# Kernel optimization log

Measured on AMD Instinct MI355X. Metric: run time of the kernel, lower is better.

The kernel has to match this reference:

```python
import jax, jax.numpy as jnp
import numpy as np

D, H, F, Z = 768, 12, 2048, 100   # d_model, nhead, dim_feedforward, d_z
NL = 2                            # num enc layers == num dec layers
RATIO = 0.05                      # filter_ratio
EPS = 1e-5


def _ln(x, g, b):
    m = x.mean(-1, keepdims=True)
    v = ((x - m) ** 2).mean(-1, keepdims=True)
    return (x - m) / jnp.sqrt(v + EPS) * g + b


def _mha(x, bias, qkv_w, qkv_b, out_w, out_b):
    # x: [N, L, D] (torch seq-first: seq=N responses, batch=L token positions)
    # bias: [L, N] float key-padding mask, ADDED to logits (torch float-mask semantics)
    N, L, _ = x.shape
    hd = D // H
    qkv = jnp.einsum('nld,ed->nle', x, qkv_w) + qkv_b
    q, k, v = jnp.split(qkv, 3, axis=-1)
    q = q.reshape(N, L, H, hd)
    k = k.reshape(N, L, H, hd)
    v = v.reshape(N, L, H, hd)
    scores = jnp.einsum('nlhd,mlhd->lhnm', q, k) / jnp.sqrt(jnp.float32(hd))
    scores = scores + bias[:, None, None, :]
    attn = jax.nn.softmax(scores, axis=-1)
    o = jnp.einsum('lhnm,mlhd->nlhd', attn, v).reshape(N, L, D)
    return o @ out_w.T + out_b


def _stack(x, bias, p):
    qkv_w, qkv_b, out_w, out_b, g1, b1, w1, c1, w2, c2, g2, b2 = p
    for i in range(NL):  # post-norm TransformerEncoderLayer, relu FFN, eval (no dropout)
        a = _mha(x, bias, qkv_w[i], qkv_b[i], out_w[i], out_b[i])
        x = _ln(x + a, g1[i], b1[i])
        f = jax.nn.relu(x @ w1[i].T + c1[i]) @ w2[i].T + c2[i]
        x = _ln(x + f, g2[i], b2[i])
    return x


def _anomaly_scores(emb, msk, enc_p, dec_p, pe_w, pe_b, pd_w, pd_b):
    bias = msk.T  # [L, N]
    h = _stack(emb, bias, enc_p)
    z = jnp.tanh(h @ pe_w.T + pe_b)
    zd = jnp.tanh(z @ pd_w.T + pd_b)
    d = _stack(zd, bias, dec_p)
    # per-response MSE between mean decoded and mean input embedding, summed over D
    return ((d.mean(axis=1) - emb.mean(axis=1)) ** 2).sum(-1)


def _forward(tree_lens, inputs_embeds, attention_mask, enc_p, dec_p, pe_w, pe_b, pd_w, pd_b):
    B, T, L, _ = inputs_embeds.shape
    tls = np.asarray(tree_lens)
    n_resp = tls - 1
    # pack ragged replies: rows 1..tree_len-1 of every tree -> [Ntot, L, D]
    b_idx = np.concatenate([np.full(n, b) for b, n in enumerate(n_resp)])
    t_idx = np.concatenate([np.arange(1, tl) for tl in tls])
    reply = inputs_embeds[b_idx, t_idx]
    masks = attention_mask[b_idx, t_idx]
    s = _anomaly_scores(reply, masks, enc_p, dec_p, pe_w, pe_b, pd_w, pd_b)  # [Ntot]
    Ntot = s.shape[0]
    # original: rank_idx = global_argsort filtered to indices < n_resp[b] (min is always 0)
    # == argsort of the FIRST n_resp[b] packed scores (faithful to the source's indexing)
    masked = jnp.where(jnp.arange(Ntot)[None, :] < jnp.asarray(n_resp)[:, None],
                       s[None, :], jnp.inf)
    order = jnp.argsort(masked, axis=1)[:, :T - 1]  # [B, T-1]
    n_ext = np.maximum(np.floor(n_resp * RATIO).astype(np.int64), 1)
    sel = np.arange(T - 1)[None, :] < n_ext[:, None]          # [B, T-1]
    selj = jnp.asarray(sel)
    node_idx = jnp.where(selj, order + 1, 0)                  # pad slots reuse src (node 0)
    node_full = jnp.concatenate([jnp.zeros((B, 1), node_idx.dtype), node_idx], axis=1)
    brow = jnp.arange(B)[:, None]
    new_emb = inputs_embeds[brow, node_full]                  # [B, T, L, D]
    valid = jnp.asarray(np.concatenate([np.ones((B, 1), bool), sel], axis=1)
                        ).astype(attention_mask.dtype)
    new_msk = attention_mask[brow, node_full] * valid[:, :, None]  # pad rows get zero mask
    ohidx = jnp.where(selj, order + 1, T)                     # dump masked scatters to col T
    oh = jnp.zeros((B, T + 1), jnp.int32).at[brow, ohidx].set(1)[:, :T].at[:, 0].set(1)
    ext_mask = jnp.repeat(oh[:, :, None], L, axis=2).reshape(B, T * L)
    new_tree_lens = jnp.asarray(1 + n_ext, dtype=jnp.int32)
    n_ext_adv = 0
    return oh, ext_mask, n_ext_adv, new_tree_lens, new_emb, new_msk


def setup_inputs() -> dict:
    B, T, L = 16, 32, 64
    key = jax.random.key(0)
    ks = list(jax.random.split(key, 4))
    inp = {
        'tree_lens': jax.random.randint(ks[0], (B,), T // 2, T + 1),
        'inputs_embeds': jax.random.normal(ks[1], (B, T, L, D), jnp.float32),
        'attention_mask': jnp.ones((B, T, L), jnp.float32),
    }
    kit = iter(jax.random.split(ks[2], 32))
    def w(shape):
        return jax.random.normal(next(kit), (NL,) + shape, jnp.float32) * 0.02
    for pre in ('enc', 'dec'):
        inp[pre + '_qkv_w'] = w((3 * D, D)); inp[pre + '_qkv_b'] = jnp.zeros((NL, 3 * D))
        inp[pre + '_out_w'] = w((D, D));     inp[pre + '_out_b'] = jnp.zeros((NL, D))
        inp[pre + '_ln1_g'] = jnp.ones((NL, D)); inp[pre + '_ln1_b'] = jnp.zeros((NL, D))
        inp[pre + '_w1'] = w((F, D)); inp[pre + '_c1'] = jnp.zeros((NL, F))
        inp[pre + '_w2'] = w((D, F)); inp[pre + '_c2'] = jnp.zeros((NL, D))
        inp[pre + '_ln2_g'] = jnp.ones((NL, D)); inp[pre + '_ln2_b'] = jnp.zeros((NL, D))
    inp['pe_w'] = jax.random.normal(next(kit), (Z, D), jnp.float32) * 0.02
    inp['pe_b'] = jnp.zeros((Z,), jnp.float32)
    inp['pd_w'] = jax.random.normal(next(kit), (D, Z), jnp.float32) * 0.02
    inp['pd_b'] = jnp.zeros((D,), jnp.float32)
    return inp


def reference(tree_lens, inputs_embeds, attention_mask,
              enc_qkv_w, enc_qkv_b, enc_out_w, enc_out_b, enc_ln1_g, enc_ln1_b,
              enc_w1, enc_c1, enc_w2, enc_c2, enc_ln2_g, enc_ln2_b,
              dec_qkv_w, dec_qkv_b, dec_out_w, dec_out_b, dec_ln1_g, dec_ln1_b,
              dec_w1, dec_c1, dec_w2, dec_c2, dec_ln2_g, dec_ln2_b,
              pe_w, pe_b, pd_w, pd_b):
    enc_p = (enc_qkv_w, enc_qkv_b, enc_out_w, enc_out_b, enc_ln1_g, enc_ln1_b,
             enc_w1, enc_c1, enc_w2, enc_c2, enc_ln2_g, enc_ln2_b)
    dec_p = (dec_qkv_w, dec_qkv_b, dec_out_w, dec_out_b, dec_ln1_g, dec_ln1_b,
             dec_w1, dec_c1, dec_w2, dec_c2, dec_ln2_g, dec_ln2_b)
    return _forward(tree_lens, inputs_embeds, attention_mask, enc_p, dec_p,
                    pe_w, pe_b, pd_w, pd_b)
```

## Files before the change

kernel.cpp:

```cpp
#include <hip/hip_runtime.h>
#include <hip/hip_bf16.h>
#include <math.h>


#define B_  16
#define T_  32
#define L_  64
#define D_  768
#define H_  12
#define F_  2048
#define ZR_ 100
#define ZP_ 128
#define NP_ 512
#define EPS_ 1e-5f

#define MI_NTOT  0
#define MI_NRESP 8
#define MI_OFF   32
#define MI_BIDX  64
#define MI_TIDX  576
#define MI_NODE  1088

#define WS_BIAS2 2048
#define WS_EMEAN 34816
#define WS_S     428032
#define WS_WST   428544
#define WS_BIG   1313280

#define OUT_OH   0
#define OUT_EXT  512
#define OUT_NEA  33280
#define OUT_NTL  33281
#define OUT_NEMB 33297
#define OUT_NMSK 25199121
#define OUT_XSCR 33300

typedef __attribute__((ext_vector_type(8))) short short8;
typedef __attribute__((ext_vector_type(4))) float f32x4;

__device__ inline float bf2f(unsigned s) {
  return __uint_as_float((s & 0xffffu) << 16);
}
__device__ inline unsigned short f2bf(float x) {
  unsigned u = __float_as_uint(x);
  u += 0x7fffu + ((u >> 16) & 1u);
  return (unsigned short)(u >> 16);
}
__device__ inline unsigned pack2(float a, float b) {
  return (unsigned)f2bf(a) | ((unsigned)f2bf(b) << 16);
}

__global__ void meta_kernel(const int* __restrict__ tl, int* __restrict__ mi) {
  if (threadIdx.x != 0) return;
  int off = 0;
  for (int b = 0; b < B_; b++) {
    int nr = tl[b] - 1;
    mi[MI_NRESP + b] = nr;
    mi[MI_OFF + b] = off;
    off += nr;
  }
  mi[MI_NTOT] = off;
  for (int j = 0; j < NP_; j++) {
    int b = -1, t = 0;
    if (j < off) {
      b = 0;
      while (b + 1 < B_ && j >= mi[MI_OFF + b + 1]) b++;
      t = j - mi[MI_OFF + b] + 1;
    }
    mi[MI_BIDX + j] = b;
    mi[MI_TIDX + j] = t;
  }
}

__global__ __launch_bounds__(256) void w2bf_kernel(const float* __restrict__ W,
                                                   unsigned short* __restrict__ o) {
  const int i = (blockIdx.x * 256 + threadIdx.x) * 4;
  float4 v = *(const float4*)(W + i);
  uint2 pk; pk.x = pack2(v.x, v.y); pk.y = pack2(v.z, v.w);
  *(uint2*)(o + i) = pk;
}

__global__ __launch_bounds__(192) void gather_kernel(
    const float* __restrict__ emb, const float* __restrict__ am,
    const int* __restrict__ mi, unsigned short* __restrict__ X,
    float* __restrict__ bias2) {
  const int blk = blockIdx.x;
  const int j = blk >> 6, l = blk & 63;
  const int ntot = mi[MI_NTOT];
  const int t = threadIdx.x;
  float4 v = make_float4(0.f, 0.f, 0.f, 0.f);
  if (j < ntot) {
    const int b = mi[MI_BIDX + j], tt = mi[MI_TIDX + j];
    v = ((const float4*)(emb + (size_t)((b * T_ + tt) * L_ + l) * D_))[t];
    if (t == 0) bias2[blk] = am[(b * T_ + tt) * L_ + l];
  } else {
    if (t == 0) bias2[blk] = -1e30f;
  }
  uint2 pk; pk.x = pack2(v.x, v.y); pk.y = pack2(v.z, v.w);
  *(uint2*)(X + (size_t)blk * D_ + t * 4) = pk;
}

__global__ __launch_bounds__(256) void emean_kernel(const unsigned short* __restrict__ X,
                                                    float* __restrict__ em) {
  const int j = blockIdx.x;
  int d = threadIdx.x;
  for (int c = 0; c < 3; c++, d += 256) {
    const unsigned short* p = X + (size_t)j * L_ * D_ + d;
    float s = 0.f;
    for (int l = 0; l < L_; l++) s += bf2f(p[l * D_]);
    em[j * D_ + d] = s * (1.f / 64.f);
  }
}

__device__ inline float blockSum256(float v, float* red) {
  #pragma unroll
  for (int o = 32; o > 0; o >>= 1) v += __shfl_down(v, o);
  const int lane = threadIdx.x & 63, wid = threadIdx.x >> 6;
  __syncthreads();
  if (lane == 0) red[wid] = v;
  __syncthreads();
  return red[0] + red[1] + red[2] + red[3];
}

__global__ __launch_bounds__(256) void ln_kernel(unsigned short* __restrict__ X,
                                                 const float* __restrict__ g,
                                                 const float* __restrict__ bb,
                                                 const int* __restrict__ mi) {
  const int row = blockIdx.x * 4 + (threadIdx.x >> 6);
  if (row >= mi[MI_NTOT] * L_) return;
  const int lane = threadIdx.x & 63;
  unsigned short* p = X + (size_t)row * D_;
  float v[12];
  #pragma unroll
  for (int c = 0; c < 3; c++) {
    uint2 u = *(const uint2*)(p + lane * 4 + c * 256);
    v[c * 4 + 0] = bf2f(u.x); v[c * 4 + 1] = bf2f(u.x >> 16);
    v[c * 4 + 2] = bf2f(u.y); v[c * 4 + 3] = bf2f(u.y >> 16);
  }
  float s = 0.f;
  #pragma unroll
  for (int i = 0; i < 12; i++) s += v[i];
  #pragma unroll
  for (int o = 32; o > 0; o >>= 1) s += __shfl_xor(s, o);
  const float m = s * (1.f / 768.f);
  float q = 0.f;
  #pragma unroll
  for (int i = 0; i < 12; i++) { v[i] -= m; q += v[i] * v[i]; }
  #pragma unroll
  for (int o = 32; o > 0; o >>= 1) q += __shfl_xor(q, o);
  const float r = rsqrtf(q * (1.f / 768.f) + EPS_);
  #pragma unroll
  for (int c = 0; c < 3; c++) {
    const int d = lane * 4 + c * 256;
    float4 gv = *(const float4*)(g + d);
    float4 bv = *(const float4*)(bb + d);
    uint2 pk;
    pk.x = pack2(v[c * 4 + 0] * r * gv.x + bv.x, v[c * 4 + 1] * r * gv.y + bv.y);
    pk.y = pack2(v[c * 4 + 2] * r * gv.z + bv.z, v[c * 4 + 3] * r * gv.w + bv.w);
    *(uint2*)(p + d) = pk;
  }
}

template <int ACT, bool ADD>
__global__ __launch_bounds__(512) void gemm_mfma(
    const unsigned short* __restrict__ A, int lda, int K,
    const unsigned short* __restrict__ W, int ldw,
    const float* __restrict__ bias,
    unsigned short* __restrict__ C, int ldc,
    const int* __restrict__ mi) {
  const int rows = mi[MI_NTOT] * 64;
  const int row0 = blockIdx.x * 256;
  if (row0 >= rows) return;
  const int col0 = blockIdx.y * 256;
  __shared__ unsigned short Sh[6 * 8192];
  unsigned short* SA = Sh;
  unsigned short* SB = Sh + 3 * 8192;
  const int t = threadIdx.x;
  const int lane = t & 63, w = t >> 6;
  const int wr = w >> 2, wc = w & 3;
  const int quad = lane >> 4, l15 = lane & 15;
  f32x4 acc[8][4];
  #pragma unroll
  for (int i = 0; i < 8; i++)
    #pragma unroll
    for (int j = 0; j < 4; j++) acc[i][j] = (f32x4){0.f, 0.f, 0.f, 0.f};

  int schunk[2];
  const unsigned short* gA[2];
  const unsigned short* gB[2];
  #pragma unroll
  for (int r = 0; r < 2; r++) {
    const int c = r * 8 + w;
    const int g = c * 64 + lane;
    const int row = g >> 2, slot = g & 3;
    const int kg = slot ^ ((row >> 1) & 3);
    schunk[r] = c;
    gA[r] = A + (size_t)(row0 + row) * lda + kg * 8;
    gB[r] = W + (size_t)(col0 + row) * ldw + kg * 8;
  }
  int aoff[8], boff[4];
  #pragma unroll
  for (int m = 0; m < 8; m++) {
    const int ar = wr * 128 + m * 16 + l15;
    aoff[m] = ar * 32 + (quad ^ ((ar >> 1) & 3)) * 8;
  }
  #pragma unroll
  for (int n = 0; n < 4; n++) {
    const int bn = wc * 64 + n * 16 + l15;
    boff[n] = bn * 32 + (quad ^ ((bn >> 1) & 3)) * 8;
  }

#define STAGE_(bi_, kk_)                                                       \
  { const int _off = (bi_) * 8192;                                             \
    _Pragma("unroll")                                                          \
    for (int r = 0; r < 2; r++) {                                              \
      __builtin_amdgcn_global_load_lds(                                        \
          (const __attribute__((address_space(1))) void*)(gA[r] + (kk_)),      \
          (__attribute__((address_space(3))) void*)(SA + _off + schunk[r] * 512), \
          16, 0, 0);                                                           \
      __builtin_amdgcn_global_load_lds(                                        \
          (const __attribute__((address_space(1))) void*)(gB[r] + (kk_)),      \
          (__attribute__((address_space(3))) void*)(SB + _off + schunk[r] * 512), \
          16, 0, 0);                                                           \
    } }

#define COMPUTE_(bi_)                                                          \
  {                                                                            \
    const int _off = (bi_) * 8192;                                             \
    short8 bfr[4];                                                             \
    _Pragma("unroll")                                                          \
    for (int n = 0; n < 4; n++) bfr[n] = *(const short8*)(SB + _off + boff[n]); \
    _Pragma("unroll")                                                          \
    for (int m = 0; m < 8; m++) {                                              \
      short8 afm = *(const short8*)(SA + _off + aoff[m]);                      \
      _Pragma("unroll")                                                        \
      for (int n = 0; n < 4; n++)                                              \
        acc[m][n] = __builtin_amdgcn_mfma_f32_16x16x32_bf16(afm, bfr[n],       \
                                                            acc[m][n], 0, 0, 0); \
    }                                                                          \
  }

  const int NS = K >> 5;
  STAGE_(0, 0);
  STAGE_(1, 32);
  int bi = 0;
  for (int i = 0; i < NS; i++) {
    if (i + 1 < NS) {
      asm volatile("s_waitcnt vmcnt(4)\ns_barrier" ::: "memory");
    } else {
      asm volatile("s_waitcnt vmcnt(0)\ns_barrier" ::: "memory");
    }
    __builtin_amdgcn_sched_barrier(0);
    if (i + 2 < NS) {
      const int b2 = (bi >= 1) ? bi - 1 : 2;
      STAGE_(b2, (i + 2) * 32);
    }
    COMPUTE_(bi);
    bi = (bi >= 2) ? 0 : bi + 1;
  }
  __syncthreads();

#undef STAGE_
#undef COMPUTE_

  unsigned short* slice = Sh + w * 4096;
  float bv[4];
  #pragma unroll
  for (int n = 0; n < 4; n++) bv[n] = bias[col0 + wc * 64 + n * 16 + l15];
  #pragma unroll
  for (int p = 0; p < 2; p++) {
    #pragma unroll
    for (int mm = 0; mm < 4; mm++) {
      #pragma unroll
      for (int reg = 0; reg < 4; reg++) {
        const int r64 = mm * 16 + quad * 4 + reg;
        #pragma unroll
        for (int n = 0; n < 4; n++) {
          float x = acc[p * 4 + mm][n][reg] + bv[n];
          if (ACT == 1) x = fmaxf(x, 0.f);
          slice[r64 * 64 + n * 16 + l15] = f2bf(x);
        }
      }
    }
    unsigned short* crow =
        C + (size_t)(row0 + wr * 128 + p * 64) * ldc + col0 + wc * 64;
    #pragma unroll
    for (int i = 0; i < 8; i++) {
      const int j = i * 64 + lane;
      const int r64 = j >> 3, c8 = (j & 7) * 8;
      short8 v = *(const short8*)(slice + j * 8);
      unsigned short* cp = crow + (size_t)r64 * ldc + c8;
      if (ADD) {
        short8 cv = *(const short8*)cp;
        #pragma unroll
        for (int e = 0; e < 8; e++)
          v[e] = (short)f2bf(bf2f((unsigned short)v[e]) +
                             bf2f((unsigned short)cv[e]));
      }
      *(short8*)cp = v;
    }
  }
}

template <int ACT, int AT, int CT>
__global__ __launch_bounds__(256) void gemm_kernel(
    const void* __restrict__ Av, int lda, int kloop,
    const float* __restrict__ W, int kw, int nreal,
    const float* __restrict__ bias,
    void* __restrict__ Cv, int ldc,
    const int* __restrict__ mi) {
  if ((int)blockIdx.x >= mi[MI_NTOT]) return;
  __shared__ float As[16][68];
  __shared__ float Ws[16][68];
  const int t = threadIdx.x;
  const int tx = t & 15, ty = t >> 4;
  const int lrow = t >> 2, lkg = (t & 3) * 4;
  const size_t row0 = (size_t)blockIdx.x * 64;
  const int col0 = blockIdx.y * 64;
  float acc[4][4] = {};
  for (int k0 = 0; k0 < kloop; k0 += 16) {
    float a4[4];
    if (AT == 0) {
      float4 av = *(const float4*)((const float*)Av + (row0 + lrow) * (size_t)lda + k0 + lkg);
      a4[0] = av.x; a4[1] = av.y; a4[2] = av.z; a4[3] = av.w;
    } else {
      uint2 u = *(const uint2*)((const unsigned short*)Av + (row0 + lrow) * (size_t)lda + k0 + lkg);
      a4[0] = bf2f(u.x); a4[1] = bf2f(u.x >> 16);
      a4[2] = bf2f(u.y); a4[3] = bf2f(u.y >> 16);
    }
    float wv[4];
    const int wn = col0 + lrow;
    #pragma unroll
    for (int i = 0; i < 4; i++) {
      const int k = k0 + lkg + i;
      wv[i] = (wn < nreal && k < kw) ? W[(size_t)wn * kw + k] : 0.f;
    }
    __syncthreads();
    As[lkg + 0][lrow] = a4[0]; As[lkg + 1][lrow] = a4[1];
    As[lkg + 2][lrow] = a4[2]; As[lkg + 3][lrow] = a4[3];
    Ws[lkg + 0][lrow] = wv[0]; Ws[lkg + 1][lrow] = wv[1];
    Ws[lkg + 2][lrow] = wv[2]; Ws[lkg + 3][lrow] = wv[3];
    __syncthreads();
    #pragma unroll
    for (int kk = 0; kk < 16; kk++) {
      float4 av4 = *(const float4*)(&As[kk][ty * 4]);
      float4 wv4 = *(const float4*)(&Ws[kk][tx * 4]);
      float aa[4] = {av4.x, av4.y, av4.z, av4.w};
      float ww[4] = {wv4.x, wv4.y, wv4.z, wv4.w};
      #pragma unroll
      for (int i = 0; i < 4; i++)
        #pragma unroll
        for (int j = 0; j < 4; j++) acc[i][j] += aa[i] * ww[j];
    }
  }
  const int n0 = col0 + tx * 4;
  float bv[4];
  #pragma unroll
  for (int j = 0; j < 4; j++) bv[j] = (n0 + j < nreal) ? bias[n0 + j] : 0.f;
  #pragma unroll
  for (int i = 0; i < 4; i++) {
    float v[4];
    #pragma unroll
    for (int j = 0; j < 4; j++) {
      float x = acc[i][j] + bv[j];
      if (ACT == 1) x = fmaxf(x, 0.f);
      if (ACT == 2) x = tanhf(x);
      v[j] = x;
    }
    if (CT == 0) {
      float* cp = (float*)Cv + (row0 + ty * 4 + i) * (size_t)ldc + n0;
      *(float4*)cp = make_float4(v[0], v[1], v[2], v[3]);
    } else {
      unsigned short* cp = (unsigned short*)Cv + (row0 + ty * 4 + i) * (size_t)ldc + n0;
      uint2 pk; pk.x = pack2(v[0], v[1]); pk.y = pack2(v[2], v[3]);
      *(uint2*)cp = pk;
    }
  }
}

__global__ __launch_bounds__(512) void attn_kernel(
    unsigned short* __restrict__ QKV, const float* __restrict__ bias2,
    const int* __restrict__ mi) {
  const int ntot = mi[MI_NTOT];
  const int l = blockIdx.x, h = blockIdx.y;
  const int ntk = (ntot + 63) >> 6;
  __shared__ unsigned short Ks[512 * 64];
  __shared__ unsigned short Vt[8 * 4096];
  __shared__ unsigned short Ps[8][1024];
  __shared__ float bs[512];
  const int t = threadIdx.x;
  const int lane = t & 63, w = t >> 6;
  const int quad = lane >> 4, l15 = lane & 15;

  {
    const int sub = lane >> 3;
    const int cc = (lane & 7) ^ sub;
    for (int it = 0; it < ntk; it++) {
      const int m = it * 64 + w * 8 + sub;
      const unsigned short* src =
          QKV + (size_t)(m * L_ + l) * 2304 + 768 + h * 64 + cc * 8;
      __builtin_amdgcn_global_load_lds(
          (const __attribute__((address_space(1))) void*)src,
          (__attribute__((address_space(3))) void*)(Ks + it * 4096 + w * 512),
          16, 0, 0);
    }
  }
  {
    const int m = t & 63;
    const int d0 = (t >> 6) * 8;
    for (int mt = 0; mt < ntk; mt++) {
      short8 v = *(const short8*)(
          QKV + (size_t)((mt * 64 + m) * L_ + l) * 2304 + 1536 + h * 64 + d0);
      #pragma unroll
      for (int i = 0; i < 8; i++) {
        const int d = d0 + i;
        Vt[mt * 4096 + d * 64 + (((m >> 3) ^ (d & 7)) * 8) + (m & 7)] =
            (unsigned short)v[i];
      }
    }
  }
  bs[t] = bias2[t * 64 + l];
  __syncthreads();

  const int nqt = (ntot + 127) >> 7;
  for (int qt = 0; qt < nqt; qt++) {
    const int qbase = qt * 128 + w * 16;
    if (qbase >= ntot) continue;

    short8 af[2];
    #pragma unroll
    for (int kc = 0; kc < 2; kc++)
      af[kc] = *(const short8*)(
          QKV + (size_t)((qbase + l15) * L_ + l) * 2304 + h * 64 + (kc * 4 + quad) * 8);

    f32x4 oa[4];
    float runmax[4], runsum[4];
    #pragma unroll
    for (int f = 0; f < 4; f++) oa[f] = (f32x4){0.f, 0.f, 0.f, 0.f};
    #pragma unroll
    for (int r2 = 0; r2 < 4; r2++) { runmax[r2] = -3.0e38f; runsum[r2] = 0.f; }

    for (int mt = 0; mt < ntk; mt++) {
      f32x4 sv[4];
      #pragma unroll
      for (int cb = 0; cb < 4; cb++) {
        sv[cb] = (f32x4){0.f, 0.f, 0.f, 0.f};
        const int mrow = mt * 64 + cb * 16 + l15;
        #pragma unroll
        for (int kc = 0; kc < 2; kc++) {
          short8 bk = *(const short8*)(
              Ks + mrow * 64 + (((kc * 4 + quad) ^ (mrow & 7)) * 8));
          sv[cb] = __builtin_amdgcn_mfma_f32_16x16x32_bf16(af[kc], bk, sv[cb], 0, 0, 0);
        }
      }

      float bj[4];
      #pragma unroll
      for (int cb = 0; cb < 4; cb++) bj[cb] = bs[mt * 64 + cb * 16 + l15];
      float pj[4][4];
      #pragma unroll
      for (int cb = 0; cb < 4; cb++)
        #pragma unroll
        for (int r2 = 0; r2 < 4; r2++) pj[cb][r2] = sv[cb][r2] * 0.125f + bj[cb];
      float tmax[4];
      #pragma unroll
      for (int r2 = 0; r2 < 4; r2++)
        tmax[r2] = fmaxf(fmaxf(pj[0][r2], pj[1][r2]), fmaxf(pj[2][r2], pj[3][r2]));
      #pragma unroll
      for (int o2 = 1; o2 < 16; o2 <<= 1)
        #pragma unroll
        for (int r2 = 0; r2 < 4; r2++) tmax[r2] = fmaxf(tmax[r2], __shfl_xor(tmax[r2], o2));
      float tsum[4];
      #pragma unroll
      for (int r2 = 0; r2 < 4; r2++) {
        const float nmax = fmaxf(runmax[r2], tmax[r2]);
        const float alpha = __expf(runmax[r2] - nmax);
        runmax[r2] = nmax;
        float s0 = 0.f;
        #pragma unroll
        for (int cb = 0; cb < 4; cb++) { pj[cb][r2] = __expf(pj[cb][r2] - nmax); s0 += pj[cb][r2]; }
        tsum[r2] = s0;
        runsum[r2] *= alpha;
        #pragma unroll
        for (int f = 0; f < 4; f++) oa[f][r2] *= alpha;
      }
      #pragma unroll
      for (int o2 = 1; o2 < 16; o2 <<= 1)
        #pragma unroll
        for (int r2 = 0; r2 < 4; r2++) tsum[r2] += __shfl_xor(tsum[r2], o2);
      #pragma unroll
      for (int r2 = 0; r2 < 4; r2++) runsum[r2] += tsum[r2];

      #pragma unroll
      for (int cb = 0; cb < 4; cb++) {
        const int m = cb * 16 + l15;
        #pragma unroll
        for (int r2 = 0; r2 < 4; r2++) {
          const int q = quad * 4 + r2;
          Ps[w][q * 64 + (((m >> 3) ^ (q & 7)) * 8) + (m & 7)] = f2bf(pj[cb][r2]);
        }
      }
      short8 pa[2];
      #pragma unroll
      for (int kc = 0; kc < 2; kc++)
        pa[kc] = *(const short8*)(
            &Ps[w][l15 * 64 + (((kc * 4 + quad) ^ (l15 & 7)) * 8)]);
      #pragma unroll
      for (int f = 0; f < 4; f++) {
        const int d = f * 16 + l15;
        #pragma unroll
        for (int kc = 0; kc < 2; kc++) {
          short8 bv = *(const short8*)(
              Vt + mt * 4096 + d * 64 + (((kc * 4 + quad) ^ (d & 7)) * 8));
          oa[f] = __builtin_amdgcn_mfma_f32_16x16x32_bf16(pa[kc], bv, oa[f], 0, 0, 0);
        }
      }
    }

    #pragma unroll
    for (int r2 = 0; r2 < 4; r2++) {
      const float inv = 1.f / runsum[r2];
      const int q = quad * 4 + r2;
      #pragma unroll
      for (int f = 0; f < 4; f++)
        Ps[w][q * 64 + f * 16 + l15] = f2bf(oa[f][r2] * inv);
    }
    #pragma unroll
    for (int i = 0; i < 2; i++) {
      const int j = lane + i * 64;
      const int q = j >> 3, c8 = j & 7;
      short8 v = *(const short8*)(&Ps[w][j * 8]);
      *(short8*)(QKV + (size_t)((qbase + q) * L_ + l) * 2304 + h * 64 + c8 * 8) = v;
    }
  }
}

__global__ __launch_bounds__(256) void score_kernel(const unsigned short* __restrict__ X,
                                                    const float* __restrict__ em,
                                                    float* __restrict__ Sv) {
  const int j = blockIdx.x;
  const int t = threadIdx.x;
  __shared__ float red[4];
  float part = 0.f;
  for (int c = 0; c < 3; c++) {
    const int d = t + c * 256;
    const unsigned short* p = X + (size_t)j * L_ * D_ + d;
    float s = 0.f;
    for (int l = 0; l < L_; l++) s += bf2f(p[l * D_]);
    const float diff = s * (1.f / 64.f) - em[j * D_ + d];
    part += diff * diff;
  }
  const float tot = blockSum256(part, red);
  if (t == 0) Sv[j] = tot;
}

__global__ __launch_bounds__(256) void finalize_kernel(const float* __restrict__ Sv,
                                                       int* __restrict__ mi,
                                                       float* __restrict__ out) {
  const int t = threadIdx.x;
  if (t < B_) {
    const int nr = mi[MI_NRESP + t];
    float best = 3.0e38f; int bi = 0;
    for (int j = 0; j < nr; j++) {
      const float v = Sv[j];
      if (v < best) { best = v; bi = j; }
    }
    mi[MI_NODE + t] = bi + 1;
    int next = nr / 20; if (next < 1) next = 1;
    out[OUT_NTL + t] = (float)(1 + next);
  }
  if (t == 0) out[OUT_NEA] = 0.f;
  __syncthreads();
  for (int idx = t; idx < B_ * T_; idx += 256) {
    const int b = idx >> 5, tt = idx & 31;
    out[OUT_OH + idx] = (tt == 0 || tt == mi[MI_NODE + b]) ? 1.f : 0.f;
  }
}

__global__ __launch_bounds__(256) void maskout_kernel(const float* __restrict__ am,
                                                      const int* __restrict__ mi,
                                                      float* __restrict__ out) {
  const int idx = blockIdx.x * 256 + threadIdx.x;
  const int b = idx >> 11, rem = idx & 2047;
  const int tt = rem >> 6, l = rem & 63;
  const int node = mi[MI_NODE + b];
  out[OUT_EXT + idx] = (tt == 0 || tt == node) ? 1.f : 0.f;
  float nm;
  if (tt == 0)      nm = am[(b * T_) * L_ + l];
  else if (tt == 1) nm = am[(b * T_ + node) * L_ + l];
  else              nm = 0.f;
  out[OUT_NMSK + idx] = nm;
}

__global__ __launch_bounds__(192) void newemb_kernel(const float* __restrict__ emb,
                                                     const int* __restrict__ mi,
                                                     float* __restrict__ out) {
  const int blk = blockIdx.x;
  const int b = blk >> 11, rem = blk & 2047;
  const int tt = rem >> 6, l = rem & 63;
  const int srct = (tt == 1) ? mi[MI_NODE + b] : 0;
  const float4 v = ((const float4*)(emb + (size_t)((b * T_ + srct) * L_ + l) * D_))[threadIdx.x];
  float* dst = out + OUT_NEMB + (size_t)blk * D_ + threadIdx.x * 4;
  dst[0] = v.x; dst[1] = v.y; dst[2] = v.z; dst[3] = v.w;
}

extern "C" void kernel_launch(void* const* d_in, const int* in_sizes, int n_in,
                              void* d_out, int out_size, void* d_ws, size_t ws_size,
                              hipStream_t stream) {
  (void)in_sizes; (void)n_in; (void)out_size; (void)ws_size;
  const int*   tl  = (const int*)d_in[0];
  const float* emb = (const float*)d_in[1];
  const float* am  = (const float*)d_in[2];
  const float* P[28];
  for (int i = 0; i < 28; i++) P[i] = (const float*)d_in[3 + i];

  float* wsf   = (float*)d_ws;
  int*   mi    = (int*)d_ws;
  float* bias2 = wsf + WS_BIAS2;
  float* emean = wsf + WS_EMEAN;
  float* Sv    = wsf + WS_S;
  unsigned short* Wst = (unsigned short*)(wsf + WS_WST);
  unsigned short* BIG = (unsigned short*)(wsf + WS_BIG);
  float* Zb    = wsf + WS_BIG;
  float* out   = (float*)d_out;
  unsigned short* X = (unsigned short*)(out + OUT_XSCR);

  meta_kernel<<<1, 64, 0, stream>>>(tl, mi);
  gather_kernel<<<NP_ * L_, 192, 0, stream>>>(emb, am, mi, X, bias2);
  emean_kernel<<<NP_, 256, 0, stream>>>(X, emean);

  const int RTM = NP_ * 64 / 256;
  const int LNB = NP_ * L_ / 4;
  for (int s = 0; s < 2; s++) {
    const float* const* q = P + s * 12;
    for (int i = 0; i < 2; i++) {
      w2bf_kernel<<<(3 * D_ * D_) / 1024, 256, 0, stream>>>(q[0] + (size_t)i * 3 * D_ * D_, Wst);
      gemm_mfma<0, false><<<dim3(RTM, 9), 512, 0, stream>>>(
          X, D_, D_, Wst, D_, q[1] + i * 3 * D_, BIG, 3 * D_, mi);
      attn_kernel<<<dim3(L_, H_), 512, 0, stream>>>(BIG, bias2, mi);
      w2bf_kernel<<<(D_ * D_) / 1024, 256, 0, stream>>>(q[2] + (size_t)i * D_ * D_, Wst);
      gemm_mfma<0, true><<<dim3(RTM, 3), 512, 0, stream>>>(
          BIG, 3 * D_, D_, Wst, D_, q[3] + i * D_, X, D_, mi);
      ln_kernel<<<LNB, 256, 0, stream>>>(X, q[4] + i * D_, q[5] + i * D_, mi);
      w2bf_kernel<<<(F_ * D_) / 1024, 256, 0, stream>>>(q[6] + (size_t)i * F_ * D_, Wst);
      gemm_mfma<1, false><<<dim3(RTM, 8), 512, 0, stream>>>(
          X, D_, D_, Wst, D_, q[7] + i * F_, BIG, F_, mi);
      w2bf_kernel<<<(D_ * F_) / 1024, 256, 0, stream>>>(q[8] + (size_t)i * D_ * F_, Wst);
      gemm_mfma<0, true><<<dim3(RTM, 3), 512, 0, stream>>>(
          BIG, F_, F_, Wst, F_, q[9] + i * D_, X, D_, mi);
      ln_kernel<<<LNB, 256, 0, stream>>>(X, q[10] + i * D_, q[11] + i * D_, mi);
    }
    if (s == 0) {
      gemm_kernel<2, 1, 0><<<dim3(NP_, 2), 256, 0, stream>>>(
          X, D_, D_, P[24], D_, ZR_, P[25], Zb, ZP_, mi);
      gemm_kernel<2, 0, 1><<<dim3(NP_, 12), 256, 0, stream>>>(
          Zb, ZP_, ZP_, P[26], ZR_, D_, P[27], X, D_, mi);
    }
  }

  score_kernel<<<NP_, 256, 0, stream>>>(X, emean, Sv);
  finalize_kernel<<<1, 256, 0, stream>>>(Sv, mi, out);
  maskout_kernel<<<128, 256, 0, stream>>>(am, mi, out);
  newemb_kernel<<<B_ * T_ * L_, 192, 0, stream>>>(emb, mi, out);
}
```

Measured before the change: 2.376 ms.

## Restructure MFMA GEMM main loop to K=64 double-buffered phased pipeline

The bf16 GEMM main loop moves from a triple-buffered K=32 scheme to a double-buffered K=64 tile with an XOR-swizzled LDS layout. Each iteration is split into four phases that issue one slice of next-tile global-to-LDS loads, read A/B fragments, then run an MFMA burst under raised wave priority (s_setprio), with barriers between phases. The aim is finer interleaving of memory traffic and matrix work with fewer loop iterations and less barrier overhead per FLOP. In exchange it uses more LDS (128KB) and adds extra barriers per iteration.

```diff
diff --git a/kernel.cpp b/kernel.cpp
--- a/kernel.cpp
+++ b/kernel.cpp
@@ -172,9 +172,7 @@
   const int row0 = blockIdx.x * 256;
   if (row0 >= rows) return;
   const int col0 = blockIdx.y * 256;
-  __shared__ unsigned short Sh[6 * 8192];
-  unsigned short* SA = Sh;
-  unsigned short* SB = Sh + 3 * 8192;
+  __shared__ unsigned short Sh[2 * 32768];
   const int t = threadIdx.x;
   const int lane = t & 63, w = t >> 6;
   const int wr = w >> 2, wc = w & 3;
@@ -185,83 +183,88 @@
     #pragma unroll
     for (int j = 0; j < 4; j++) acc[i][j] = (f32x4){0.f, 0.f, 0.f, 0.f};
 
-  int schunk[2];
-  const unsigned short* gA[2];
-  const unsigned short* gB[2];
-  #pragma unroll
-  for (int r = 0; r < 2; r++) {
-    const int c = r * 8 + w;
-    const int g = c * 64 + lane;
-    const int row = g >> 2, slot = g & 3;
-    const int kg = slot ^ ((row >> 1) & 3);
-    schunk[r] = c;
-    gA[r] = A + (size_t)(row0 + row) * lda + kg * 8;
-    gB[r] = W + (size_t)(col0 + row) * ldw + kg * 8;
-  }
-  int aoff[8], boff[4];
-  #pragma unroll
-  for (int m = 0; m < 8; m++) {
-    const int ar = wr * 128 + m * 16 + l15;
-    aoff[m] = ar * 32 + (quad ^ ((ar >> 1) & 3)) * 8;
-  }
-  #pragma unroll
-  for (int n = 0; n < 4; n++) {
-    const int bn = wc * 64 + n * 16 + l15;
-    boff[n] = bn * 32 + (quad ^ ((bn >> 1) & 3)) * 8;
-  }
-
-#define STAGE_(bi_, kk_)                                                       \
-  { const int _off = (bi_) * 8192;                                             \
+  const int sr  = w * 8 + (lane >> 3);
+  const int cc8 = ((lane & 7) ^ (lane >> 3)) * 8;
+
+  int aoffm[8], boffn[4];
+  #pragma unroll
+  for (int m = 0; m < 8; m++) aoffm[m] = (wr * 128 + m * 16 + l15) * 64;
+  #pragma unroll
+  for (int n = 0; n < 4; n++) boffn[n] = (wc * 64 + n * 16 + l15) * 64;
+  const int e7 = l15 & 7;
+  const int pq0 = ((quad)     ^ e7) * 8;
+  const int pq1 = ((4 + quad) ^ e7) * 8;
+
+#define STG(bi_, mat_, h_, kt_)                                                \
+  { const unsigned short* gp_ = (mat_) ? W : A;                                \
+    const int ld_ = (mat_) ? ldw : lda;                                        \
+    const int b0_ = (mat_) ? col0 : row0;                                      \
     _Pragma("unroll")                                                          \
-    for (int r = 0; r < 2; r++) {                                              \
+    for (int j_ = 0; j_ < 2; j_++) {                                           \
+      const unsigned short* src_ =                                             \
+          gp_ + (size_t)(b0_ + (h_) * 128 + j_ * 64 + sr) * ld_ +              \
+          (kt_) * 64 + cc8;                                                    \
       __builtin_amdgcn_global_load_lds(                                        \
-          (const __attribute__((address_space(1))) void*)(gA[r] + (kk_)),      \
-          (__attribute__((address_space(3))) void*)(SA + _off + schunk[r] * 512), \
-          16, 0, 0);                                                           \
-      __builtin_amdgcn_global_load_lds(                                        \
-          (const __attribute__((address_space(1))) void*)(gB[r] + (kk_)),      \
-          (__attribute__((address_space(3))) void*)(SB + _off + schunk[r] * 512), \
+          (const __attribute__((address_space(1))) void*)src_,                 \
+          (__attribute__((address_space(3))) void*)(Sh + (bi_) * 32768 +       \
+              (mat_) * 16384 + (h_) * 8192 + j_ * 4096 + w * 512),             \
           16, 0, 0);                                                           \
     } }
 
-#define COMPUTE_(bi_)                                                          \
-  {                                                                            \
-    const int _off = (bi_) * 8192;                                             \
-    short8 bfr[4];                                                             \
-    _Pragma("unroll")                                                          \
-    for (int n = 0; n < 4; n++) bfr[n] = *(const short8*)(SB + _off + boff[n]); \
-    _Pragma("unroll")                                                          \
-    for (int m = 0; m < 8; m++) {                                              \
-      short8 afm = *(const short8*)(SA + _off + aoff[m]);                      \
-      _Pragma("unroll")                                                        \
-      for (int n = 0; n < 4; n++)                                              \
-        acc[m][n] = __builtin_amdgcn_mfma_f32_16x16x32_bf16(afm, bfr[n],       \
-                                                            acc[m][n], 0, 0, 0); \
-    }                                                                          \
-  }
-
-  const int NS = K >> 5;
-  STAGE_(0, 0);
-  STAGE_(1, 32);
-  int bi = 0;
-  for (int i = 0; i < NS; i++) {
-    if (i + 1 < NS) {
-      asm volatile("s_waitcnt vmcnt(4)\ns_barrier" ::: "memory");
-    } else {
-      asm volatile("s_waitcnt vmcnt(0)\ns_barrier" ::: "memory");
-    }
-    __builtin_amdgcn_sched_barrier(0);
-    if (i + 2 < NS) {
-      const int b2 = (bi >= 1) ? bi - 1 : 2;
-      STAGE_(b2, (i + 2) * 32);
-    }
-    COMPUTE_(bi);
-    bi = (bi >= 2) ? 0 : bi + 1;
+  const int NT = K >> 6;
+  STG(0, 0, 0, 0); STG(0, 0, 1, 0); STG(0, 1, 0, 0); STG(0, 1, 1, 0);
+
+  for (int kt = 0; kt < NT; kt++) {
+    const int cur = kt & 1, nxt = cur ^ 1;
+    const unsigned short* SA = Sh + cur * 32768;
+    const unsigned short* SB = SA + 16384;
+    const bool more = (kt + 1 < NT);
+    short8 bfr[4][2];
+    #pragma unroll
+    for (int p = 0; p < 4; p++) {
+      if (more) {
+        if      (p == 0) STG(nxt, 0, 0, kt + 1)
+        else if (p == 1) STG(nxt, 0, 1, kt + 1)
+        else if (p == 2) STG(nxt, 1, 0, kt + 1)
+        else             STG(nxt, 1, 1, kt + 1)
+      }
+      if (p == 0) {
+        if (more) asm volatile("s_waitcnt vmcnt(2)" ::: "memory");
+        else      asm volatile("s_waitcnt vmcnt(0)" ::: "memory");
+        __builtin_amdgcn_s_barrier();
+      }
+      short8 afr[2][2];
+      if (p == 0) {
+        #pragma unroll
+        for (int n = 0; n < 4; n++) {
+          bfr[n][0] = *(const short8*)(SB + boffn[n] + pq0);
+          bfr[n][1] = *(const short8*)(SB + boffn[n] + pq1);
+        }
+      }
+      #pragma unroll
+      for (int i = 0; i < 2; i++) {
+        afr[i][0] = *(const short8*)(SA + aoffm[2 * p + i] + pq0);
+        afr[i][1] = *(const short8*)(SA + aoffm[2 * p + i] + pq1);
+      }
+      if (p != 0) __builtin_amdgcn_s_barrier();
+      asm volatile("s_waitcnt lgkmcnt(0)" ::: "memory");
+      __builtin_amdgcn_sched_barrier(0);
+      __builtin_amdgcn_s_setprio(1);
+      #pragma unroll
+      for (int i = 0; i < 2; i++)
+        #pragma unroll
+        for (int n = 0; n < 4; n++) {
+          acc[2 * p + i][n] = __builtin_amdgcn_mfma_f32_16x16x32_bf16(
+              afr[i][0], bfr[n][0], acc[2 * p + i][n], 0, 0, 0);
+          acc[2 * p + i][n] = __builtin_amdgcn_mfma_f32_16x16x32_bf16(
+              afr[i][1], bfr[n][1], acc[2 * p + i][n], 0, 0, 0);
+        }
+      __builtin_amdgcn_s_setprio(0);
+      __builtin_amdgcn_s_barrier();
+    }
   }
   __syncthreads();
-
-#undef STAGE_
-#undef COMPUTE_
+#undef STG
 
   unsigned short* slice = Sh + w * 4096;
   float bv[4];
```

Result: faster. 2.302 ms (-3.1%).
